# Performance work log

Hardware: AMD Instinct MI355X
Metric: run time of the kernel (lower is better)

The kernel has to match this reference:

```python
import jax, jax.numpy as jnp
import numpy as np

N, C = 4194304, 10
EPS = 1e-10
FOCAL_EPS = 1e-8
TEMP, THETA = 0.01, 0.1
NUM_TH = 21


def setup_inputs() -> dict:
    key = jax.random.key(0)
    k1, k2 = jax.random.split(key)
    logits = jax.random.normal(k1, (N, C), dtype=jnp.float32)
    probs = jax.nn.softmax(logits, axis=1)
    labels = jax.random.randint(k2, (N,), 0, C)
    y = jax.nn.one_hot(labels, C, dtype=jnp.float32)
    return {"probs": probs, "y": y}


def _soft_T(e):
    # sigmoid( (1/temp) * log( e*(1-theta) / clamp((1-e)*theta, eps) ) )
    num = e * (1.0 - THETA)
    den = jnp.maximum((1.0 - e) * THETA, EPS)
    frac = jnp.maximum(num / den, EPS)
    return jax.nn.sigmoid(jnp.log(frac) / TEMP)


def reference(probs, y):
    entmax = jnp.log(jnp.asarray(C, dtype=probs.dtype))
    predictions = jnp.argmax(probs, axis=1)             # [N]
    labels = jnp.argmax(y)                              # scalar (flattened argmax, as in torch code)

    # predictive uncertainty (type=0): entropy of probs per-sample
    unc = -jnp.sum(probs * jnp.log(jnp.maximum(probs, EPS)), axis=1)  # [N]

    th_list = jnp.linspace(0.0, 1.0, NUM_TH, dtype=probs.dtype)       # [21]
    umin, umax = jnp.min(unc), jnp.max(unc)
    unc_th = umin + th_list * (umax - umin)                           # [21]

    s = _soft_T(unc / entmax)                                         # [N]
    t = jnp.tanh(unc)                                                 # [N]
    w_cert = (1.0 - s) * (1.0 - t)   # weight when counted as 'certain'
    w_unc = s * t                    # weight when counted as 'uncertain'

    acc = (predictions == labels).astype(probs.dtype)                 # [N]
    inacc = 1.0 - acc

    le = (unc[None, :] <= unc_th[:, None]).astype(probs.dtype)        # [21, N]
    gt = 1.0 - le

    # one parallel masked-reduction pass over all 21 thresholds
    n_ac = le @ (acc * w_cert)
    n_au = gt @ (acc * w_unc)
    n_ic = le @ (inacc * w_cert)
    n_iu = gt @ (inacc * w_unc)

    avu = (n_ac + n_iu) / (n_ac + n_au + n_ic + n_iu + EPS)           # [21]

    # trapezoid rule over increasing th_list (direction = +1)
    dx = jnp.diff(th_list)
    auc_avu = jnp.sum((avu[1:] + avu[:-1]) * 0.5 * dx)

    # FocalLoss(gamma=1)
    logp = jnp.log(jnp.maximum(probs, FOCAL_EPS))
    ce_per = -jnp.sum(y * logp, axis=1)
    focal_per = -jnp.sum(y * logp * (1.0 - probs), axis=1)
    focal_loss = jnp.mean(focal_per)
    ce_loss = jnp.mean(ce_per)

    beta = 1.0
    savu_loss = -beta * jnp.log(jnp.maximum(auc_avu, EPS)) + focal_loss
    return (savu_loss, ce_loss)
```

## Files before the change

kernel.cpp:

```cpp
#include <hip/hip_runtime.h>

#define C 10
#define TILE 512

__device__ __forceinline__ float waveSum(float v) {
#pragma unroll
  for (int o = 32; o > 0; o >>= 1) v += __shfl_down(v, o, 64);
  return v;
}
__device__ __forceinline__ float waveMin(float v) {
#pragma unroll
  for (int o = 32; o > 0; o >>= 1) v = fminf(v, __shfl_down(v, o, 64));
  return v;
}
__device__ __forceinline__ float waveMax(float v) {
#pragma unroll
  for (int o = 32; o > 0; o >>= 1) v = fmaxf(v, __shfl_down(v, o, 64));
  return v;
}
__device__ __forceinline__ unsigned waveMaxU(unsigned v) {
#pragma unroll
  for (int o = 32; o > 0; o >>= 1) {
    unsigned w = (unsigned)__shfl_down((int)v, o, 64);
    v = v > w ? v : w;
  }
  return v;
}

#define GLD16(gp, lp)                                             \
  __builtin_amdgcn_global_load_lds(                               \
      (__attribute__((address_space(1))) void*)(gp),              \
      (__attribute__((address_space(3))) void*)(lp), 16, 0, 0)

__global__ __launch_bounds__(256, 6) void pass1(
    const float* __restrict__ probs, const float* __restrict__ y,
    float* __restrict__ us,
    unsigned* __restrict__ uminInvSlots, unsigned* __restrict__ umaxSlots,
    float* __restrict__ ceSlots, float* __restrict__ focalSlots) {
  __shared__ float buf[TILE * C];
  __shared__ float red[16];
  const int tid = threadIdx.x;
  const size_t base = (size_t)blockIdx.x * (TILE * C);

#pragma unroll
  for (int k = 0; k < 5; ++k) {
    int idx = k * 256 + tid;
    GLD16(probs + base + (size_t)idx * 4, (float*)buf + idx * 4);
  }

  int label0 = 0;
  {
    float m = y[0];
#pragma unroll
    for (int c = 1; c < C; ++c) {
      float v = y[c];
      if (v > m) { m = v; label0 = c; }
    }
  }
  __syncthreads();

  float P0[C], P1[C];
  {
    const float2* b2 = (const float2*)buf;
#pragma unroll
    for (int j = 0; j < 5; ++j) {
      float2 v = b2[tid * 5 + j];
      P0[2 * j] = v.x; P0[2 * j + 1] = v.y;
    }
#pragma unroll
    for (int j = 0; j < 5; ++j) {
      float2 v = b2[(tid + 256) * 5 + j];
      P1[2 * j] = v.x; P1[2 * j + 1] = v.y;
    }
  }
  int am0 = 0, am1 = 0;
  float m0 = P0[0], m1 = P1[0];
#pragma unroll
  for (int c = 1; c < C; ++c) {
    if (P0[c] > m0) { m0 = P0[c]; am0 = c; }
    if (P1[c] > m1) { m1 = P1[c]; am1 = c; }
  }
  float u0 = 0.f, u1 = 0.f;
#pragma unroll
  for (int c = 0; c < C; ++c) {
    u0 -= P0[c] * __logf(fmaxf(P0[c], 1e-10f));
    u1 -= P1[c] * __logf(fmaxf(P1[c], 1e-10f));
  }

  __syncthreads();
#pragma unroll
  for (int k = 0; k < 5; ++k) {
    int idx = k * 256 + tid;
    GLD16(y + base + (size_t)idx * 4, (float*)buf + idx * 4);
  }
  __syncthreads();

  float pl0 = 0.f, pl1 = 0.f;
  {
    const float2* b2 = (const float2*)buf;
#pragma unroll
    for (int j = 0; j < 5; ++j) {
      float2 v = b2[tid * 5 + j];
      pl0 = fmaf(v.x, P0[2 * j], pl0);
      pl0 = fmaf(v.y, P0[2 * j + 1], pl0);
    }
#pragma unroll
    for (int j = 0; j < 5; ++j) {
      float2 v = b2[(tid + 256) * 5 + j];
      pl1 = fmaf(v.x, P1[2 * j], pl1);
      pl1 = fmaf(v.y, P1[2 * j + 1], pl1);
    }
  }
  float ce0 = -__logf(fmaxf(pl0, 1e-8f)), ce1 = -__logf(fmaxf(pl1, 1e-8f));
  float fo0 = ce0 * (1.f - pl0), fo1 = ce1 * (1.f - pl1);

  size_t rowBase = (size_t)blockIdx.x * TILE;
  us[rowBase + tid] =
      __uint_as_float(__float_as_uint(u0) | ((am0 == label0) ? 0u : 0x80000000u));
  us[rowBase + 256 + tid] =
      __uint_as_float(__float_as_uint(u1) | ((am1 == label0) ? 0u : 0x80000000u));

  float ce = ce0 + ce1, fo = fo0 + fo1;
  float mn = fminf(u0, u1), mx = fmaxf(u0, u1);
  ce = waveSum(ce); fo = waveSum(fo);
  mn = waveMin(mn); mx = waveMax(mx);
  int wid = tid >> 6, lane = tid & 63;
  if (lane == 0) { red[wid] = ce; red[4 + wid] = fo; red[8 + wid] = mn; red[12 + wid] = mx; }
  __syncthreads();
  if (tid == 0) {
    float tce = red[0] + red[1] + red[2] + red[3];
    float tfo = red[4] + red[5] + red[6] + red[7];
    float tmn = fminf(fminf(red[8], red[9]), fminf(red[10], red[11]));
    float tmx = fmaxf(fmaxf(red[12], red[13]), fmaxf(red[14], red[15]));
    int slot = blockIdx.x & 63;
    atomicAdd(&ceSlots[slot], tce);
    atomicAdd(&focalSlots[slot], tfo);
    atomicMax(&uminInvSlots[slot], ~__float_as_uint(tmn));
    atomicMax(&umaxSlots[slot], __float_as_uint(tmx));
  }
}

__global__ __launch_bounds__(256, 4) void pass2(
    const float4* __restrict__ us4, int n4,
    const unsigned* __restrict__ uminInvSlots, const unsigned* __restrict__ umaxSlots,
    float* __restrict__ ghist) {
  __shared__ float hist[88 * 64];
  __shared__ float smm[2];
  const int tid = threadIdx.x, lane = tid & 63;
  for (int i = tid; i < 88 * 64; i += 256) hist[i] = 0.f;
  if (tid < 64) {
    unsigned mnInv = waveMaxU(uminInvSlots[tid]);
    unsigned mxb = waveMaxU(umaxSlots[tid]);
    if (tid == 0) { smm[0] = __uint_as_float(~mnInv); smm[1] = __uint_as_float(mxb); }
  }
  __syncthreads();
  const float umin = smm[0], delta = smm[1] - smm[0];
  float th[21];
#pragma unroll
  for (int k = 0; k < 21; ++k) th[k] = fmaf(0.05f * (float)k, delta, umin);

  const int stride = gridDim.x * 256;
  for (int i = blockIdx.x * 256 + tid; i < n4; i += stride) {
    float4 v = us4[i];
    float vv[4] = {v.x, v.y, v.z, v.w};
#pragma unroll
    for (int q = 0; q < 4; ++q) {
      unsigned b = __float_as_uint(vv[q]);
      int rb = (b >> 31) ? 44 : 0;
      float u = __uint_as_float(b & 0x7fffffffu);
      float e = u * 0.4342944819f;
      float lnum = __logf(e * 0.9f);
      float lden = __logf(fmaxf((1.f - e) * 0.1f, 1e-10f));
      float x = fmaxf(lnum - lden, -23.0258509f) * 100.f;
      float s = __builtin_amdgcn_rcpf(1.f + __expf(-x));
      float t = 1.f - 2.f * __builtin_amdgcn_rcpf(__expf(2.f * u) + 1.f);
      float wc = (1.f - s) * (1.f - t), wu = s * t;
      int j = 0;
#pragma unroll
      for (int k = 0; k < 21; ++k) j += (u > th[k]) ? 1 : 0;
      atomicAdd(&hist[(rb + j) * 64 + lane], wc);
      atomicAdd(&hist[(rb + 22 + j) * 64 + lane], wu);
    }
  }
  __syncthreads();
#pragma unroll
  for (int st = 32; st >= 1; st >>= 1) {
    for (int idx = tid; idx < 88 * st; idx += 256) {
      int r = idx / st, c = idx - r * st;
      hist[r * 64 + c] += hist[r * 64 + c + st];
    }
    __syncthreads();
  }
  int slot = blockIdx.x & 63;
  for (int r = tid; r < 88; r += 256)
    atomicAdd(&ghist[slot * 88 + r], hist[r * 64]);
}

__global__ __launch_bounds__(256) void pass3(
    const float* __restrict__ ghist,
    const float* __restrict__ ceSlots, const float* __restrict__ focalSlots,
    float* __restrict__ out, float invN) {
  __shared__ float hr[88];
  __shared__ float scf[2];
  int tid = threadIdx.x;
  if (tid < 88) {
    float s = 0.f;
    for (int q = 0; q < 64; ++q) s += ghist[q * 88 + tid];
    hr[tid] = s;
  }
  if (tid >= 128 && tid < 192) {
    int l = tid - 128;
    float ce = waveSum(ceSlots[l]);
    float fo = waveSum(focalSlots[l]);
    if (l == 0) { scf[0] = ce; scf[1] = fo; }
  }
  __syncthreads();
  if (tid == 0) {
    float H0[22], H1[22], H2[22], H3[22];
    float totAU = 0.f, totIU = 0.f;
    for (int j = 0; j < 22; ++j) {
      H0[j] = hr[j]; H1[j] = hr[22 + j]; H2[j] = hr[44 + j]; H3[j] = hr[66 + j];
      totAU += H1[j]; totIU += H3[j];
    }
    float n_ac = 0.f, n_ic = 0.f, n_au = totAU, n_iu = totIU;
    float auc = 0.f, prev = 0.f;
    for (int k = 0; k < 21; ++k) {
      n_ac += H0[k]; n_ic += H2[k];
      n_au -= H1[k]; n_iu -= H3[k];
      float avu = (n_ac + n_iu) / (n_ac + n_au + n_ic + n_iu + 1e-10f);
      if (k > 0) auc += (avu + prev) * 0.5f * 0.05f;
      prev = avu;
    }
    out[0] = -logf(fmaxf(auc, 1e-10f)) + scf[1] * invN;
    out[1] = scf[0] * invN;
  }
}

extern "C" void kernel_launch(void* const* d_in, const int* in_sizes, int n_in,
                              void* d_out, int out_size, void* d_ws, size_t ws_size,
                              hipStream_t stream) {
  const float* probs = (const float*)d_in[0];
  const float* y = (const float*)d_in[1];
  float* out = (float*)d_out;
  const int N = in_sizes[0] / C;

  float* wsf = (float*)d_ws;
  unsigned* uminInvSlots = (unsigned*)wsf;
  unsigned* umaxSlots = (unsigned*)(wsf + 64);
  float* ceSlots = wsf + 128;
  float* focalSlots = wsf + 192;
  float* ghist = wsf + 256;
  float* us = wsf + 5888;

  hipMemsetAsync(d_ws, 0, 5888 * sizeof(float), stream);

  pass1<<<N / TILE, 256, 0, stream>>>(probs, y, us, uminInvSlots, umaxSlots,
                                      ceSlots, focalSlots);
  pass2<<<1024, 256, 0, stream>>>((const float4*)us, N / 4, uminInvSlots, umaxSlots,
                                  ghist);
  pass3<<<1, 256, 0, stream>>>(ghist, ceSlots, focalSlots, out, 1.0f / (float)N);
}
```

Measured before the change: 387.9 us.

## Make pass1 persistent with per-wave double-buffered async LDS loads

Rewrites pass1 as a persistent kernel with a fixed grid of 128-thread blocks. Each wave owns 128-row chunks and prefetches the next chunk's probs and y into a second LDS buffer with global_load_lds while it computes the current one. Block-wide barriers between the probs and y phases are removed, and per-wave partials are accumulated across chunks before one reduction per block. The aim is to overlap memory latency with compute and cut barrier and launch overhead. The cost is far fewer resident waves per CU, and the code depends on the compiler inserting the correct wait before LDS reads.

Measured after the change: 406.4 us. +4.7%, slower.

```diff
diff --git a/kernel.cpp b/kernel.cpp
--- a/kernel.cpp
+++ b/kernel.cpp
@@ -1,7 +1,8 @@
 #include <hip/hip_runtime.h>
 
 #define C 10
-#define TILE 512
+#define CHUNK_ROWS 128
+#define CHUNK_FLOATS 1280
 
 __device__ __forceinline__ float waveSum(float v) {
 #pragma unroll
@@ -32,21 +33,20 @@
       (__attribute__((address_space(1))) void*)(gp),              \
       (__attribute__((address_space(3))) void*)(lp), 16, 0, 0)
 
-__global__ __launch_bounds__(256, 6) void pass1(
+__global__ __launch_bounds__(128, 2) void pass1(
     const float* __restrict__ probs, const float* __restrict__ y,
-    float* __restrict__ us,
+    float2* __restrict__ us2,
     unsigned* __restrict__ uminInvSlots, unsigned* __restrict__ umaxSlots,
-    float* __restrict__ ceSlots, float* __restrict__ focalSlots) {
-  __shared__ float buf[TILE * C];
-  __shared__ float red[16];
+    float* __restrict__ ceSlots, float* __restrict__ focalSlots,
+    int nchunks) {
+  __shared__ float lds[2 * 2 * 2 * CHUNK_FLOATS];
+  __shared__ float red[8];
   const int tid = threadIdx.x;
-  const size_t base = (size_t)blockIdx.x * (TILE * C);
-
-#pragma unroll
-  for (int k = 0; k < 5; ++k) {
-    int idx = k * 256 + tid;
-    GLD16(probs + base + (size_t)idx * 4, (float*)buf + idx * 4);
-  }
+  const int widx = tid >> 6, lane = tid & 63;
+  float* const wbase = lds + widx * (4 * CHUNK_FLOATS);
+
+  const int gw = blockIdx.x * 2 + widx;
+  const int NW = gridDim.x * 2;
 
   int label0 = 0;
   {
@@ -57,81 +57,75 @@
       if (v > m) { m = v; label0 = c; }
     }
   }
-  __syncthreads();
-
-  float P0[C], P1[C];
-  {
-    const float2* b2 = (const float2*)buf;
-#pragma unroll
-    for (int j = 0; j < 5; ++j) {
-      float2 v = b2[tid * 5 + j];
-      P0[2 * j] = v.x; P0[2 * j + 1] = v.y;
-    }
-#pragma unroll
-    for (int j = 0; j < 5; ++j) {
-      float2 v = b2[(tid + 256) * 5 + j];
-      P1[2 * j] = v.x; P1[2 * j + 1] = v.y;
-    }
-  }
-  int am0 = 0, am1 = 0;
-  float m0 = P0[0], m1 = P1[0];
-#pragma unroll
-  for (int c = 1; c < C; ++c) {
-    if (P0[c] > m0) { m0 = P0[c]; am0 = c; }
-    if (P1[c] > m1) { m1 = P1[c]; am1 = c; }
-  }
-  float u0 = 0.f, u1 = 0.f;
-#pragma unroll
-  for (int c = 0; c < C; ++c) {
-    u0 -= P0[c] * __logf(fmaxf(P0[c], 1e-10f));
-    u1 -= P1[c] * __logf(fmaxf(P1[c], 1e-10f));
-  }
-
-  __syncthreads();
-#pragma unroll
-  for (int k = 0; k < 5; ++k) {
-    int idx = k * 256 + tid;
-    GLD16(y + base + (size_t)idx * 4, (float*)buf + idx * 4);
-  }
-  __syncthreads();
-
-  float pl0 = 0.f, pl1 = 0.f;
-  {
-    const float2* b2 = (const float2*)buf;
-#pragma unroll
-    for (int j = 0; j < 5; ++j) {
-      float2 v = b2[tid * 5 + j];
-      pl0 = fmaf(v.x, P0[2 * j], pl0);
-      pl0 = fmaf(v.y, P0[2 * j + 1], pl0);
-    }
-#pragma unroll
-    for (int j = 0; j < 5; ++j) {
-      float2 v = b2[(tid + 256) * 5 + j];
-      pl1 = fmaf(v.x, P1[2 * j], pl1);
-      pl1 = fmaf(v.y, P1[2 * j + 1], pl1);
-    }
-  }
-  float ce0 = -__logf(fmaxf(pl0, 1e-8f)), ce1 = -__logf(fmaxf(pl1, 1e-8f));
-  float fo0 = ce0 * (1.f - pl0), fo1 = ce1 * (1.f - pl1);
-
-  size_t rowBase = (size_t)blockIdx.x * TILE;
-  us[rowBase + tid] =
-      __uint_as_float(__float_as_uint(u0) | ((am0 == label0) ? 0u : 0x80000000u));
-  us[rowBase + 256 + tid] =
-      __uint_as_float(__float_as_uint(u1) | ((am1 == label0) ? 0u : 0x80000000u));
-
-  float ce = ce0 + ce1, fo = fo0 + fo1;
-  float mn = fminf(u0, u1), mx = fmaxf(u0, u1);
-  ce = waveSum(ce); fo = waveSum(fo);
-  mn = waveMin(mn); mx = waveMax(mx);
-  int wid = tid >> 6, lane = tid & 63;
-  if (lane == 0) { red[wid] = ce; red[4 + wid] = fo; red[8 + wid] = mn; red[12 + wid] = mx; }
+
+  auto issue = [&](int c, int b) {
+    const size_t g = (size_t)c * CHUNK_FLOATS + (size_t)lane * 4;
+    float* lp = wbase + b * (2 * CHUNK_FLOATS);
+#pragma unroll
+    for (int q = 0; q < 5; ++q)
+      GLD16(probs + g + q * 256, lp + q * 256 + lane * 4);
+#pragma unroll
+    for (int q = 0; q < 5; ++q)
+      GLD16(y + g + q * 256, lp + CHUNK_FLOATS + q * 256 + lane * 4);
+  };
+
+  float ceA = 0.f, foA = 0.f;
+  float mnA = __uint_as_float(0x7f800000u), mxA = 0.f;
+
+  if (gw < nchunks) issue(gw, 0);
+  int b = 0;
+  for (int c = gw; c < nchunks; c += NW, b ^= 1) {
+    if (c + NW < nchunks) issue(c + NW, b ^ 1);
+
+    const float4* pp = (const float4*)(wbase + b * (2 * CHUNK_FLOATS));
+    const float4* yy = (const float4*)(wbase + b * (2 * CHUNK_FLOATS) + CHUNK_FLOATS);
+    float P[20], Yv[20];
+#pragma unroll
+    for (int q = 0; q < 5; ++q) {
+      float4 v = pp[lane * 5 + q];
+      P[4 * q] = v.x; P[4 * q + 1] = v.y; P[4 * q + 2] = v.z; P[4 * q + 3] = v.w;
+    }
+#pragma unroll
+    for (int q = 0; q < 5; ++q) {
+      float4 v = yy[lane * 5 + q];
+      Yv[4 * q] = v.x; Yv[4 * q + 1] = v.y; Yv[4 * q + 2] = v.z; Yv[4 * q + 3] = v.w;
+    }
+
+    int am0 = 0, am1 = 0;
+    float m0 = P[0], m1 = P[10];
+#pragma unroll
+    for (int cc = 1; cc < C; ++cc) {
+      if (P[cc] > m0) { m0 = P[cc]; am0 = cc; }
+      if (P[10 + cc] > m1) { m1 = P[10 + cc]; am1 = cc; }
+    }
+    float u0 = 0.f, u1 = 0.f, pl0 = 0.f, pl1 = 0.f;
+#pragma unroll
+    for (int cc = 0; cc < C; ++cc) {
+      u0 -= P[cc] * __logf(fmaxf(P[cc], 1e-10f));
+      u1 -= P[10 + cc] * __logf(fmaxf(P[10 + cc], 1e-10f));
+      pl0 = fmaf(Yv[cc], P[cc], pl0);
+      pl1 = fmaf(Yv[10 + cc], P[10 + cc], pl1);
+    }
+    float ce0 = -__logf(fmaxf(pl0, 1e-8f)), ce1 = -__logf(fmaxf(pl1, 1e-8f));
+    ceA += ce0 + ce1;
+    foA += ce0 * (1.f - pl0) + ce1 * (1.f - pl1);
+    mnA = fminf(mnA, fminf(u0, u1));
+    mxA = fmaxf(mxA, fmaxf(u0, u1));
+
+    unsigned s0 = __float_as_uint(u0) | ((am0 == label0) ? 0u : 0x80000000u);
+    unsigned s1 = __float_as_uint(u1) | ((am1 == label0) ? 0u : 0x80000000u);
+    us2[(size_t)c * 64 + lane] = make_float2(__uint_as_float(s0), __uint_as_float(s1));
+  }
+
+  float ce = waveSum(ceA), fo = waveSum(foA);
+  float mn = waveMin(mnA), mx = waveMax(mxA);
+  if (lane == 0) { red[widx] = ce; red[2 + widx] = fo; red[4 + widx] = mn; red[6 + widx] = mx; }
   __syncthreads();
   if (tid == 0) {
-    float tce = red[0] + red[1] + red[2] + red[3];
-    float tfo = red[4] + red[5] + red[6] + red[7];
-    float tmn = fminf(fminf(red[8], red[9]), fminf(red[10], red[11]));
-    float tmx = fmaxf(fmaxf(red[12], red[13]), fmaxf(red[14], red[15]));
+    float tce = red[0] + red[1];
+    float tfo = red[2] + red[3];
+    float tmn = fminf(red[4], red[5]);
+    float tmx = fmaxf(red[6], red[7]);
     int slot = blockIdx.x & 63;
     atomicAdd(&ceSlots[slot], tce);
     atomicAdd(&focalSlots[slot], tfo);
@@ -254,8 +248,9 @@
 
   hipMemsetAsync(d_ws, 0, 5888 * sizeof(float), stream);
 
-  pass1<<<N / TILE, 256, 0, stream>>>(probs, y, us, uminInvSlots, umaxSlots,
-                                      ceSlots, focalSlots);
+  const int nchunks = N / CHUNK_ROWS;
+  pass1<<<1024, 128, 0, stream>>>(probs, y, (float2*)us, uminInvSlots, umaxSlots,
+                                  ceSlots, focalSlots, nchunks);
   pass2<<<1024, 256, 0, stream>>>((const float4*)us, N / 4, uminInvSlots, umaxSlots,
                                   ghist);
   pass3<<<1, 256, 0, stream>>>(ghist, ceSlots, focalSlots, out, 1.0f / (float)N);
```
